# Performance work log

Hardware: AMD Instinct MI355X
Metric: run time of the kernel (lower is better)

Reference implementation:

```python
import jax, jax.numpy as jnp
import numpy as np

GAMMA = 0.95        # gamma_lemma: persistence decay per cycle (eq. 12.1)
KAPPA = 0.1         # kappa_interfere: lateral interference strength (eq. 12.3)
T_STEPS = 50        # t_lemma_steps: integration window before selection (eq. 12.2)
FLOOR = 1e-6        # confidence_floor for peak-to-average ratio

B, N_CONCEPTS, N_LEMMAS = 4096, 1024, 512


def setup_inputs() -> dict:
    key = jax.random.key(0)
    k1, k2 = jax.random.split(key, 2)
    # kernel boundary hands in a normalized concept distribution
    c_raw = jax.random.uniform(k1, (B, N_CONCEPTS), dtype=jnp.float32)
    c_lex = c_raw / jnp.sum(c_raw, axis=-1, keepdims=True)
    # TiedSubstrate W_C_to_L: (out_dim=n_lemmas, in_dim=n_concepts)
    W = jax.random.normal(k2, (N_LEMMAS, N_CONCEPTS), dtype=jnp.float32) / np.sqrt(N_CONCEPTS)
    # persistent lemma activation buffer a_lemma, zero at reset
    a0 = jnp.zeros((B, N_LEMMAS), dtype=jnp.float32)
    return {"c_lex": c_lex, "W": W, "a0": a0}


def reference(c_lex, W, a0):
    """Integrate lemma activations for T_STEPS cycles, then select.

    Per cycle (eq. 12.1 + 12.3):
      a <- gamma * a + c_lex @ W^T            # decay + concept->lemma drive
      a <- a - kappa * (sum_j a_j - a)        # lateral interference from other lemmas
      a <- max(a, 0)                          # rectify activations
    Selection (eq. 12.2): argmax over lemmas; confidence = peak / max(mean, floor).
    """
    def step(a, _):
        a = GAMMA * a + jnp.einsum('bc,lc->bl', c_lex, W)   # (B, n_lemmas)
        a = a - KAPPA * (jnp.sum(a, axis=-1, keepdims=True) - a)
        a = jnp.maximum(a, 0.0)
        return a, None

    a, _ = jax.lax.scan(step, a0, None, length=T_STEPS)
    peak = jnp.max(a, axis=-1)
    mean = jnp.mean(a, axis=-1)
    confidence = peak / jnp.maximum(mean, FLOOR)
    selected = jnp.argmax(a, axis=-1)
    return a, selected, confidence
```

## Files before the change

kernel.cpp:

```cpp
#include <hip/hip_runtime.h>
#include <hip/hip_bf16.h>

#define BATCH 4096
#define NC    1024
#define NL    512
#define TSTEPS 50
#define GAMMA_C 0.95f
#define KAPPA_C 0.1f
#define FLOOR_C 1e-6f

typedef __attribute__((ext_vector_type(8))) short short8;
typedef __attribute__((ext_vector_type(4))) float f32x4;

__device__ __forceinline__ void split2_pk(float x0, float x1,
                                          unsigned& hp, unsigned& lp) {
    union { __hip_bfloat162 b; unsigned u; } ch, cl;
    ch.b = __float22bfloat162_rn(make_float2(x0, x1));
    hp = ch.u;
    const float hf0 = __uint_as_float(hp << 16);
    const float hf1 = __uint_as_float(hp & 0xFFFF0000u);
    cl.b = __float22bfloat162_rn(make_float2(x0 - hf0, x1 - hf1));
    lp = cl.u;
}

#define W_FLOATS (NL * NC)
#define W_BLOCKS (W_FLOATS / (256 * 8))
#define A_BLOCKS ((BATCH * NC) / (256 * 8))

__global__ __launch_bounds__(256)
void convert_hilo(const float* __restrict__ W, const float* __restrict__ A,
                  unsigned short* __restrict__ Whi, unsigned short* __restrict__ Wlo,
                  unsigned short* __restrict__ Ahi, unsigned short* __restrict__ Alo) {
    const int b = blockIdx.x;
    const float* src;
    unsigned short *dh, *dl;
    if (b < W_BLOCKS) {
        const size_t fidx = ((size_t)b * 256 + threadIdx.x) * 8;
        src = W + fidx; dh = Whi + fidx; dl = Wlo + fidx;
    } else {
        const size_t fidx = ((size_t)(b - W_BLOCKS) * 256 + threadIdx.x) * 8;
        src = A + fidx; dh = Ahi + fidx; dl = Alo + fidx;
    }
    const float4 v0 = ((const float4*)src)[0];
    const float4 v1 = ((const float4*)src)[1];
    uint4 h, l;
    split2_pk(v0.x, v0.y, h.x, l.x);
    split2_pk(v0.z, v0.w, h.y, l.y);
    split2_pk(v1.x, v1.y, h.z, l.z);
    split2_pk(v1.z, v1.w, h.w, l.w);
    *(uint4*)dh = h;
    *(uint4*)dl = l;
}

__device__ __forceinline__ float wave_sum_bcast(float x) {
    float f = x;
    f += __int_as_float(__builtin_amdgcn_update_dpp(
            0, __float_as_int(f), 0x111, 0xf, 0xf, true));
    f += __int_as_float(__builtin_amdgcn_update_dpp(
            0, __float_as_int(f), 0x112, 0xf, 0xf, true));
    f += __int_as_float(__builtin_amdgcn_update_dpp(
            0, __float_as_int(f), 0x114, 0xf, 0xf, true));
    f += __int_as_float(__builtin_amdgcn_update_dpp(
            0, __float_as_int(f), 0x118, 0xf, 0xf, true));
    f += __int_as_float(__builtin_amdgcn_update_dpp(
            0, __float_as_int(f), 0x142, 0xa, 0xf, true));
    f += __int_as_float(__builtin_amdgcn_update_dpp(
            0, __float_as_int(f), 0x143, 0xc, 0xf, true));
    return __int_as_float(__builtin_amdgcn_readlane(__float_as_int(f), 63));
}

#define TM 128
#define TN 128
#define GK 32
#define NST 8

__device__ __forceinline__ void glds16(const unsigned short* g, unsigned short* l) {
    __builtin_amdgcn_global_load_lds(
        (__attribute__((address_space(1))) void*)(g),
        (__attribute__((address_space(3))) void*)(l), 16, 0, 0);
}

__global__ __launch_bounds__(256)
void gemm_bf16x2(const unsigned short* __restrict__ Ahi, const unsigned short* __restrict__ Alo,
                 const unsigned short* __restrict__ Whi, const unsigned short* __restrict__ Wlo,
                 float* __restrict__ Dp) {
    __shared__ unsigned short S[2][4][TM * GK];

    const int tid  = threadIdx.x;
    const int lane = tid & 63;
    const int w    = tid >> 6;
    const int m0 = blockIdx.x * TM;
    const int n0 = blockIdx.y * TN;
    const int kb = blockIdx.z * (GK * NST);

    const int srow = w * 32 + (lane >> 2);
    const int scol = (lane & 3) * 8;
    const unsigned short* gAh = Ahi + (size_t)(m0 + srow) * NC + kb + scol;
    const unsigned short* gAl = Alo + (size_t)(m0 + srow) * NC + kb + scol;
    const unsigned short* gBh = Whi + (size_t)(n0 + srow) * NC + kb + scol;
    const unsigned short* gBl = Wlo + (size_t)(n0 + srow) * NC + kb + scol;
    const int ld0 = (w * 32) * GK + lane * 8;

    const int mw   = (w >> 1) * 64;
    const int nw   = (w & 1) * 64;
    const int sr   = lane & 15;
    const int quad = lane >> 4;
    const int rA = (mw + sr) * GK + quad * 8;
    const int rB = (nw + sr) * GK + quad * 8;

    f32x4 acc[4][4];
    #pragma unroll
    for (int i = 0; i < 4; ++i)
        #pragma unroll
        for (int j = 0; j < 4; ++j)
            acc[i][j] = (f32x4){0.f, 0.f, 0.f, 0.f};

    #define STAGE(buf, kofs)                                          \
        {                                                             \
            const int ko = (kofs);                                    \
            glds16(gAh + ko,           &S[buf][0][ld0]);              \
            glds16(gAh + ko + 16 * NC, &S[buf][0][ld0 + 16 * GK]);    \
            glds16(gAl + ko,           &S[buf][1][ld0]);              \
            glds16(gAl + ko + 16 * NC, &S[buf][1][ld0 + 16 * GK]);    \
            glds16(gBh + ko,           &S[buf][2][ld0]);              \
            glds16(gBh + ko + 16 * NC, &S[buf][2][ld0 + 16 * GK]);    \
            glds16(gBl + ko,           &S[buf][3][ld0]);              \
            glds16(gBl + ko + 16 * NC, &S[buf][3][ld0 + 16 * GK]);    \
        }

    STAGE(0, 0);
    __syncthreads();

    #pragma unroll
    for (int s = 0; s < NST; ++s) {
        const int cur = s & 1;
        if (s + 1 < NST)
            STAGE(cur ^ 1, (s + 1) * GK);

        short8 afh[4], afl[4], bfh[4], bfl[4];
        #pragma unroll
        for (int mi = 0; mi < 4; ++mi) {
            afh[mi] = *(const short8*)&S[cur][0][rA + mi * 16 * GK];
            afl[mi] = *(const short8*)&S[cur][1][rA + mi * 16 * GK];
        }
        #pragma unroll
        for (int ni = 0; ni < 4; ++ni) {
            bfh[ni] = *(const short8*)&S[cur][2][rB + ni * 16 * GK];
            bfl[ni] = *(const short8*)&S[cur][3][rB + ni * 16 * GK];
        }

        #pragma unroll
        for (int mi = 0; mi < 4; ++mi) {
            #pragma unroll
            for (int ni = 0; ni < 4; ++ni) {
                acc[mi][ni] = __builtin_amdgcn_mfma_f32_16x16x32_bf16(
                    afh[mi], bfh[ni], acc[mi][ni], 0, 0, 0);
                acc[mi][ni] = __builtin_amdgcn_mfma_f32_16x16x32_bf16(
                    afh[mi], bfl[ni], acc[mi][ni], 0, 0, 0);
                acc[mi][ni] = __builtin_amdgcn_mfma_f32_16x16x32_bf16(
                    afl[mi], bfh[ni], acc[mi][ni], 0, 0, 0);
            }
        }
        __syncthreads();
    }

    float* Dz = Dp + (size_t)blockIdx.z * BATCH * NL;
    #pragma unroll
    for (int mi = 0; mi < 4; ++mi) {
        #pragma unroll
        for (int ni = 0; ni < 4; ++ni) {
            const int col = n0 + nw + ni * 16 + sr;
            #pragma unroll
            for (int r = 0; r < 4; ++r) {
                const int row = m0 + mw + mi * 16 + quad * 4 + r;
                Dz[(size_t)row * NL + col] = acc[mi][ni][r];
            }
        }
    }
}

template<int SK>
__global__ __launch_bounds__(256)
void iterate_select(const float* __restrict__ Dp,
                    float* __restrict__ a_out,
                    float* __restrict__ sel_out, float* __restrict__ conf_out) {
    const int lane = threadIdx.x & 63;
    const int wave = threadIdx.x >> 6;
    const int row  = blockIdx.x * 4 + wave;

    float d[8];
    {
        float4 v[SK][2];
        #pragma unroll
        for (int s = 0; s < SK; ++s) {
            const float4* ps = (const float4*)(Dp + (size_t)s * BATCH * NL
                                               + (size_t)row * NL + lane * 8);
            v[s][0] = ps[0];
            v[s][1] = ps[1];
        }
        d[0] = v[0][0].x; d[1] = v[0][0].y; d[2] = v[0][0].z; d[3] = v[0][0].w;
        d[4] = v[0][1].x; d[5] = v[0][1].y; d[6] = v[0][1].z; d[7] = v[0][1].w;
        #pragma unroll
        for (int s = 1; s < SK; ++s) {
            d[0] += v[s][0].x; d[1] += v[s][0].y; d[2] += v[s][0].z; d[3] += v[s][0].w;
            d[4] += v[s][1].x; d[5] += v[s][1].y; d[6] += v[s][1].z; d[7] += v[s][1].w;
        }
    }

    float a[8];
    #pragma unroll
    for (int j = 0; j < 8; ++j) a[j] = 0.f;

    const float K1 = 1.0f + KAPPA_C;

    for (int t = 0; t < TSTEPS; ++t) {
        #pragma unroll
        for (int j = 0; j < 8; ++j) a[j] = fmaf(GAMMA_C, a[j], d[j]);

        float t4a = a[0] + a[4], t4b = a[1] + a[5], t4c = a[2] + a[6], t4d = a[3] + a[7];
        float t2a = t4a + t4c, t2b = t4b + t4d;
        const float S = wave_sum_bcast(t2a + t2b);

        const float h = -KAPPA_C * S;
        #pragma unroll
        for (int j = 0; j < 8; ++j) {
            const float v = fmaf(K1, a[j], h);
            a[j] = v > 0.f ? v : 0.f;
        }
    }

    float m4a = fmaxf(a[0], a[4]), m4b = fmaxf(a[1], a[5]);
    float m4c = fmaxf(a[2], a[6]), m4d = fmaxf(a[3], a[7]);
    float peak = fmaxf(fmaxf(m4a, m4b), fmaxf(m4c, m4d));
    float s4a = a[0] + a[4], s4b = a[1] + a[5], s4c = a[2] + a[6], s4d = a[3] + a[7];
    float ssum = wave_sum_bcast((s4a + s4b) + (s4c + s4d));

    #pragma unroll
    for (int m = 1; m < 64; m <<= 1)
        peak = fmaxf(peak, __shfl_xor(peak, m, 64));

    const float mean = ssum * (1.0f / (float)NL);
    const float conf = peak / fmaxf(mean, FLOOR_C);

    int idx = 0x7fffffff;
    #pragma unroll
    for (int j = 0; j < 8; ++j)
        if (a[j] == peak) idx = min(idx, lane * 8 + j);
    #pragma unroll
    for (int m = 1; m < 64; m <<= 1)
        idx = min(idx, __shfl_xor(idx, m, 64));

    float4* ar = (float4*)(a_out + (size_t)row * NL + lane * 8);
    float4 o0, o1;
    o0.x = a[0]; o0.y = a[1]; o0.z = a[2]; o0.w = a[3];
    o1.x = a[4]; o1.y = a[5]; o1.z = a[6]; o1.w = a[7];
    ar[0] = o0; ar[1] = o1;

    if (lane == 0) {
        if (sel_out)  sel_out[row]  = (float)idx;
        if (conf_out) conf_out[row] = conf;
    }
}

extern "C" void kernel_launch(void* const* d_in, const int* in_sizes, int n_in,
                              void* d_out, int out_size, void* d_ws, size_t ws_size,
                              hipStream_t stream) {
    const float* c_lex = (const float*)d_in[0];
    const float* W     = (const float*)d_in[1];

    float* D = (float*)d_ws;
    unsigned short* Whi = (unsigned short*)(D + 4ull * BATCH * NL);
    unsigned short* Wlo = Whi + (size_t)NL * NC;
    unsigned short* Ahi = Wlo + (size_t)NL * NC;
    unsigned short* Alo = Ahi + (size_t)BATCH * NC;

    float* a_out = (float*)d_out;
    float* sel   = nullptr;
    float* conf  = nullptr;
    const int base = BATCH * NL;
    if (out_size >= base + 2 * BATCH) {
        sel  = a_out + base;
        conf = a_out + base + BATCH;
    } else if (out_size >= base + BATCH) {
        conf = a_out + base;
    }

    convert_hilo<<<dim3(W_BLOCKS + A_BLOCKS), 256, 0, stream>>>(
        W, c_lex, Whi, Wlo, Ahi, Alo);

    gemm_bf16x2<<<dim3(BATCH / TM, NL / TN, 4), 256, 0, stream>>>(
        Ahi, Alo, Whi, Wlo, D);

    iterate_select<4><<<dim3(BATCH / 4), 256, 0, stream>>>(D, a_out, sel, conf);
}
```

Baseline: 109.0 us.

## Halve split-K and restructure GEMM k-loop with explicit vmcnt-gated double buffering

Reduces the split-K factor from 4 to 2, so each GEMM block covers twice the K range and fewer partial-sum planes are written and later read by the iterate kernel. The k-loop is rewritten as a macro step that waits on vmcnt for the current stage, uses raw s_barrier with sched_barriers, and refills the just-consumed buffer after compute, keeping two stages in flight. The goal is less partial-sum memory traffic and better overlap of global-to-LDS loads with MFMA work, at the cost of fewer blocks (256 rather than 512) and hand-managed wait counts that must stay correct.

```diff
diff --git a/kernel.cpp b/kernel.cpp
--- a/kernel.cpp
+++ b/kernel.cpp
@@ -69,16 +69,17 @@
     return __int_as_float(__builtin_amdgcn_readlane(__float_as_int(f), 63));
 }
 
-#define TM 128
-#define TN 128
-#define GK 32
-#define NST 8
-
 __device__ __forceinline__ void glds16(const unsigned short* g, unsigned short* l) {
     __builtin_amdgcn_global_load_lds(
         (__attribute__((address_space(1))) void*)(g),
         (__attribute__((address_space(3))) void*)(l), 16, 0, 0);
 }
+
+#define TM 128
+#define TN 128
+#define GK 32
+#define SPLITK 2
+#define NST (NC / SPLITK / GK)
 
 __global__ __launch_bounds__(256)
 void gemm_bf16x2(const unsigned short* __restrict__ Ahi, const unsigned short* __restrict__ Alo,
@@ -91,7 +92,7 @@
     const int w    = tid >> 6;
     const int m0 = blockIdx.x * TM;
     const int n0 = blockIdx.y * TN;
-    const int kb = blockIdx.z * (GK * NST);
+    const int kb = blockIdx.z * (NC / SPLITK);
 
     const int srow = w * 32 + (lane >> 2);
     const int scol = (lane & 3) * 8;
@@ -128,41 +129,49 @@
             glds16(gBl + ko + 16 * NC, &S[buf][3][ld0 + 16 * GK]);    \
         }
 
+    #define KSTEP(CUR, VM, DO_STAGE, NEXTK)                                    \
+        {                                                                      \
+            asm volatile("s_waitcnt vmcnt(" #VM ")" ::: "memory");             \
+            __builtin_amdgcn_sched_barrier(0);                                 \
+            __builtin_amdgcn_s_barrier();                                      \
+            __builtin_amdgcn_sched_barrier(0);                                 \
+            short8 afh[4], afl[4], bfh[4], bfl[4];                             \
+            _Pragma("unroll")                                                  \
+            for (int mi = 0; mi < 4; ++mi) {                                   \
+                afh[mi] = *(const short8*)&S[CUR][0][rA + mi * 16 * GK];       \
+                afl[mi] = *(const short8*)&S[CUR][1][rA + mi * 16 * GK];       \
+            }                                                                  \
+            _Pragma("unroll")                                                  \
+            for (int ni = 0; ni < 4; ++ni) {                                   \
+                bfh[ni] = *(const short8*)&S[CUR][2][rB + ni * 16 * GK];       \
+                bfl[ni] = *(const short8*)&S[CUR][3][rB + ni * 16 * GK];       \
+            }                                                                  \
+            _Pragma("unroll")                                                  \
+            for (int mi = 0; mi < 4; ++mi) {                                   \
+                _Pragma("unroll")                                              \
+                for (int ni = 0; ni < 4; ++ni) {                               \
+                    acc[mi][ni] = __builtin_amdgcn_mfma_f32_16x16x32_bf16(     \
+                        afh[mi], bfh[ni], acc[mi][ni], 0, 0, 0);               \
+                    acc[mi][ni] = __builtin_amdgcn_mfma_f32_16x16x32_bf16(     \
+                        afh[mi], bfl[ni], acc[mi][ni], 0, 0, 0);               \
+                    acc[mi][ni] = __builtin_amdgcn_mfma_f32_16x16x32_bf16(     \
+                        afl[mi], bfh[ni], acc[mi][ni], 0, 0, 0);               \
+                }                                                              \
+            }                                                                  \
+            __builtin_amdgcn_sched_barrier(0);                                 \
+            __builtin_amdgcn_s_barrier();                                      \
+            __builtin_amdgcn_sched_barrier(0);                                 \
+            if (DO_STAGE) STAGE(CUR, NEXTK);                                   \
+        }
+
     STAGE(0, 0);
-    __syncthreads();
-
-    #pragma unroll
-    for (int s = 0; s < NST; ++s) {
-        const int cur = s & 1;
-        if (s + 1 < NST)
-            STAGE(cur ^ 1, (s + 1) * GK);
-
-        short8 afh[4], afl[4], bfh[4], bfl[4];
-        #pragma unroll
-        for (int mi = 0; mi < 4; ++mi) {
-            afh[mi] = *(const short8*)&S[cur][0][rA + mi * 16 * GK];
-            afl[mi] = *(const short8*)&S[cur][1][rA + mi * 16 * GK];
-        }
-        #pragma unroll
-        for (int ni = 0; ni < 4; ++ni) {
-            bfh[ni] = *(const short8*)&S[cur][2][rB + ni * 16 * GK];
-            bfl[ni] = *(const short8*)&S[cur][3][rB + ni * 16 * GK];
-        }
-
-        #pragma unroll
-        for (int mi = 0; mi < 4; ++mi) {
-            #pragma unroll
-            for (int ni = 0; ni < 4; ++ni) {
-                acc[mi][ni] = __builtin_amdgcn_mfma_f32_16x16x32_bf16(
-                    afh[mi], bfh[ni], acc[mi][ni], 0, 0, 0);
-                acc[mi][ni] = __builtin_amdgcn_mfma_f32_16x16x32_bf16(
-                    afh[mi], bfl[ni], acc[mi][ni], 0, 0, 0);
-                acc[mi][ni] = __builtin_amdgcn_mfma_f32_16x16x32_bf16(
-                    afl[mi], bfh[ni], acc[mi][ni], 0, 0, 0);
-            }
-        }
-        __syncthreads();
-    }
+    STAGE(1, GK);
+
+    #pragma unroll 2
+    for (int s = 0; s < NST - 2; ++s)
+        KSTEP((s & 1), 8, true, (s + 2) * GK);
+    KSTEP(0, 8, false, 0);
+    KSTEP(1, 0, false, 0);
 
     float* Dz = Dp + (size_t)blockIdx.z * BATCH * NL;
     #pragma unroll
@@ -269,7 +278,7 @@
     const float* W     = (const float*)d_in[1];
 
     float* D = (float*)d_ws;
-    unsigned short* Whi = (unsigned short*)(D + 4ull * BATCH * NL);
+    unsigned short* Whi = (unsigned short*)(D + (size_t)SPLITK * BATCH * NL);
     unsigned short* Wlo = Whi + (size_t)NL * NC;
     unsigned short* Ahi = Wlo + (size_t)NL * NC;
     unsigned short* Alo = Ahi + (size_t)BATCH * NC;
@@ -288,8 +297,8 @@
     convert_hilo<<<dim3(W_BLOCKS + A_BLOCKS), 256, 0, stream>>>(
         W, c_lex, Whi, Wlo, Ahi, Alo);
 
-    gemm_bf16x2<<<dim3(BATCH / TM, NL / TN, 4), 256, 0, stream>>>(
+    gemm_bf16x2<<<dim3(BATCH / TM, NL / TN, SPLITK), 256, 0, stream>>>(
         Ahi, Alo, Whi, Wlo, D);
 
-    iterate_select<4><<<dim3(BATCH / 4), 256, 0, stream>>>(D, a_out, sel, conf);
-}
+    iterate_select<SPLITK><<<dim3(BATCH / 4), 256, 0, stream>>>(D, a_out, sel, conf);
+}
```

New measurement: 109.8 us. No clear change (+0.8%).
